# Kernel optimization log

Measured on AMD Instinct MI355X. Metric: run time of the kernel, lower is better.

Reference implementation:

```python
import jax, jax.numpy as jnp
import numpy as np

NEG_SLOPE = 0.01
H = 128  # hidden_conv_1 == hidden_conv_2


def leaky(x):
    return jnp.where(x >= 0, x, NEG_SLOPE * x)


def gru_cell(x, h, w_ih, w_hh, b_ih, b_hh):
    # PyTorch GRUCell: gates stacked [r, z, n] along dim 0 of w_ih/w_hh
    gi = x @ w_ih.T + b_ih  # [N, 3H]
    gh = h @ w_hh.T + b_hh
    ir, iz, inn = jnp.split(gi, 3, axis=-1)
    hr, hz, hn = jnp.split(gh, 3, axis=-1)
    r = jax.nn.sigmoid(ir + hr)
    z = jax.nn.sigmoid(iz + hz)
    n = jnp.tanh(inn + r * hn)
    return (1.0 - z) * n + z * h


def gcn_conv(x, w, b, src, dst, num_nodes):
    # PyG GCNConv: add self-loops, symmetric normalization, linear first
    xw = x @ w.T  # [N, H]
    loop = jnp.arange(num_nodes, dtype=src.dtype)
    s = jnp.concatenate([src, loop])
    d = jnp.concatenate([dst, loop])
    deg = jax.ops.segment_sum(jnp.ones_like(d, dtype=x.dtype), d, num_segments=num_nodes)
    dinv = jnp.where(deg > 0, jax.lax.rsqrt(deg), 0.0)
    norm = dinv[s] * dinv[d]  # [E+N]
    msg = xw[s] * norm[:, None]
    out = jax.ops.segment_sum(msg, d, num_segments=num_nodes)
    return out + b


def setup_inputs() -> dict:
    key = jax.random.key(0)
    ks = jax.random.split(key, 24)
    N, E, EL, IN_DIM, OUT_DIM = 100000, 600000, 200000, 128, 2

    def lin(k, fan_in, fan_out):
        k1, k2 = jax.random.split(k)
        bound = 1.0 / np.sqrt(fan_in)
        w = jax.random.uniform(k1, (fan_out, fan_in), minval=-bound, maxval=bound, dtype=jnp.float32)
        b = jax.random.uniform(k2, (fan_out,), minval=-bound, maxval=bound, dtype=jnp.float32)
        return w, b

    w_pre1, b_pre1 = lin(ks[0], IN_DIM, 256)
    w_pre2, b_pre2 = lin(ks[1], 256, H)
    w_c1, b_c1 = lin(ks[2], H, H)
    w_c2, b_c2 = lin(ks[3], H, H)
    w_post, b_post = lin(ks[4], H, OUT_DIM)

    def gru_params(k):
        k1, k2, k3, k4 = jax.random.split(k, 4)
        bound = 1.0 / np.sqrt(H)
        u = lambda kk, shape: jax.random.uniform(kk, shape, minval=-bound, maxval=bound, dtype=jnp.float32)
        return u(k1, (3 * H, H)), u(k2, (3 * H, H)), u(k3, (3 * H,)), u(k4, (3 * H,))

    g1_wih, g1_whh, g1_bih, g1_bhh = gru_params(ks[5])
    g2_wih, g2_whh, g2_bih, g2_bhh = gru_params(ks[6])

    x = jax.random.normal(ks[7], (N, IN_DIM), dtype=jnp.float32)
    edge_index = jax.random.randint(ks[8], (2, E), 0, N, dtype=jnp.int64 if jax.config.jax_enable_x64 else jnp.int32)
    edge_label_index = jax.random.randint(ks[9], (2, EL), 0, N, dtype=edge_index.dtype)
    prev_emb0 = jax.random.normal(ks[10], (N, H), dtype=jnp.float32)
    prev_emb1 = jax.random.normal(ks[11], (N, H), dtype=jnp.float32)

    return {
        'x': x, 'edge_index': edge_index, 'edge_label_index': edge_label_index,
        'prev_emb0': prev_emb0, 'prev_emb1': prev_emb1,
        'w_pre1': w_pre1, 'b_pre1': b_pre1, 'w_pre2': w_pre2, 'b_pre2': b_pre2,
        'w_c1': w_c1, 'b_c1': b_c1, 'w_c2': w_c2, 'b_c2': b_c2,
        'w_post': w_post, 'b_post': b_post,
        'g1_wih': g1_wih, 'g1_whh': g1_whh, 'g1_bih': g1_bih, 'g1_bhh': g1_bhh,
        'g2_wih': g2_wih, 'g2_whh': g2_whh, 'g2_bih': g2_bih, 'g2_bhh': g2_bhh,
    }


def reference(x, edge_index, edge_label_index, prev_emb0, prev_emb1,
              w_pre1, b_pre1, w_pre2, b_pre2, w_c1, b_c1, w_c2, b_c2,
              w_post, b_post, g1_wih, g1_whh, g1_bih, g1_bhh,
              g2_wih, g2_whh, g2_bih, g2_bhh):
    N = x.shape[0]
    src, dst = edge_index[0], edge_index[1]

    # preprocess (dropout p=0.0 -> identity)
    h = leaky(x @ w_pre1.T + b_pre1)
    h = leaky(h @ w_pre2.T + b_pre2)

    # unconditional GRU fuse with previous 0-hop embedding (detached in torch)
    h = jax.lax.stop_gradient(gru_cell(h, prev_emb0, g1_wih, g1_whh, g1_bih, g1_bhh))
    emb0 = h

    h = leaky(gcn_conv(h, w_c1, b_c1, src, dst, N))
    h = jax.lax.stop_gradient(gru_cell(h, prev_emb0, g1_wih, g1_whh, g1_bih, g1_bhh))
    emb1 = h

    h = leaky(gcn_conv(h, w_c2, b_c2, src, dst, N))
    h = jax.lax.stop_gradient(gru_cell(h, prev_emb1, g2_wih, g2_whh, g2_bih, g2_bhh))
    emb2 = h

    # LP head: gather + hadamard + linear + sum
    h_src = h[edge_label_index[0]]
    h_dst = h[edge_label_index[1]]
    logits = jnp.sum((h_src * h_dst) @ w_post.T + b_post, axis=-1)  # [EL]
    return logits, emb0, emb1, emb2
```

## Files before the change

### kernel.cpp

```cpp
#include <hip/hip_runtime.h>
#include <hip/hip_bf16.h>
#include <type_traits>


typedef __bf16 bf16;
typedef __bf16 bf16x8 __attribute__((ext_vector_type(8)));
typedef float  f32x4  __attribute__((ext_vector_type(4)));

#define DEV __device__ __forceinline__

DEV f32x4 mfma16(bf16x8 a, bf16x8 b, f32x4 c) {
    return __builtin_amdgcn_mfma_f32_16x16x32_bf16(a, b, c, 0, 0, 0);
}

DEV bf16x8 load_a8(const float* p) {
    f32x4 lo = *(const f32x4*)p;
    f32x4 hi = *(const f32x4*)(p + 4);
    bf16x8 v;
    v[0] = (bf16)lo[0]; v[1] = (bf16)lo[1]; v[2] = (bf16)lo[2]; v[3] = (bf16)lo[3];
    v[4] = (bf16)hi[0]; v[5] = (bf16)hi[1]; v[6] = (bf16)hi[2]; v[7] = (bf16)hi[3];
    return v;
}
DEV bf16x8 load_a8(const bf16* p) { return *(const bf16x8*)p; }

__global__ void cvt_kernel(const float* __restrict__ in, bf16* __restrict__ ob, int n) {
    const int i = blockIdx.x * 256 + threadIdx.x;
    if (i < n) ob[i] = (bf16)in[i];
}

template<int Ci, int Co, bool ACT, bool BIAS, typename AT, typename OT>
__global__ __launch_bounds__(256) void gemm_kernel(
    const AT* __restrict__ A, const bf16* __restrict__ W,
    const float* __restrict__ bias, OT* __restrict__ C, int M)
{
    const int tid  = threadIdx.x;
    const int lane = tid & 63, w = tid >> 6;
    const int lr   = lane & 15, ko = lane >> 4;
    const int rbase = blockIdx.x * 64 + w * 16;

    long arow = rbase + lr; if (arow > M - 1) arow = M - 1;
    constexpr int KC = Ci / 32;
    constexpr int NT = Co / 16;

    bf16x8 a[KC];
#pragma unroll
    for (int kc = 0; kc < KC; ++kc)
        a[kc] = load_a8(A + arow * Ci + kc * 32 + ko * 8);

#pragma unroll
    for (int t = 0; t < NT; ++t) {
        f32x4 acc = {0.f, 0.f, 0.f, 0.f};
        const bf16* wp = W + (long)(t * 16 + lr) * Ci + ko * 8;
#pragma unroll
        for (int kc = 0; kc < KC; ++kc)
            acc = mfma16(a[kc], *(const bf16x8*)(wp + kc * 32), acc);

        const int col = t * 16 + lr;
        float bv = 0.f;
        if (BIAS) bv = bias[col];
#pragma unroll
        for (int j = 0; j < 4; ++j) {
            const int orow = rbase + ko * 4 + j;
            if (orow < M) {
                float v = acc[j] + bv;
                if (ACT) v = (v >= 0.f) ? v : 0.01f * v;
                C[(long)orow * Co + col] = (OT)v;
            }
        }
    }
}

template<typename XT>
__global__ __launch_bounds__(256) void gru_kernel(
    const XT* x, const float* __restrict__ hp,
    const bf16* __restrict__ wih, const bf16* __restrict__ whh,
    const float* __restrict__ bih, const float* __restrict__ bhh,
    float* out, int N)
{
    __shared__ bf16 Lw[6][16][128];

    const int tid  = threadIdx.x;
    const int lane = tid & 63, w = tid >> 6;
    const int lr   = lane & 15, ko = lane >> 4;
    const long rbase = (long)blockIdx.x * 64 + w * 16;

    long arow = rbase + lr; if (arow > N - 1) arow = N - 1;
    bf16x8 ax[4], ah[4];
#pragma unroll
    for (int kc = 0; kc < 4; ++kc) {
        ax[kc] = load_a8(x  + arow * 128 + kc * 32 + ko * 8);
        ah[kc] = load_a8(hp + arow * 128 + kc * 32 + ko * 8);
    }

    for (int tc = 0; tc < 8; ++tc) {
        __syncthreads();
#pragma unroll
        for (int i = 0; i < 6; ++i) {
            const int ch  = tid + 256 * i;
            const int g   = ch >> 8, rem = ch & 255;
            const int row = rem >> 4, cc = rem & 15;
            const int scc = cc ^ (row & 7);
            const bf16* wsrc = (g < 3 ? wih : whh)
                + (long)(((g % 3) * 128 + tc * 16 + row) * 128 + scc * 8);
            *(bf16x8*)(&Lw[g][row][cc * 8]) = *(const bf16x8*)wsrc;
        }
        __syncthreads();

        const int col = tc * 16 + lr;
        const float br = bih[col]       + bhh[col];
        const float bz = bih[128 + col] + bhh[128 + col];
        const float bi = bih[256 + col];
        const float bh = bhh[256 + col];

        f32x4 ar = {0.f, 0.f, 0.f, 0.f};
        f32x4 az = {0.f, 0.f, 0.f, 0.f};
        f32x4 ai = {0.f, 0.f, 0.f, 0.f};
        f32x4 ag = {0.f, 0.f, 0.f, 0.f};
#pragma unroll
        for (int kc = 0; kc < 4; ++kc) {
            const int cc = (kc * 4 + ko) ^ (lr & 7);
            bf16x8 wr_i = *(const bf16x8*)(&Lw[0][lr][cc * 8]);
            bf16x8 wz_i = *(const bf16x8*)(&Lw[1][lr][cc * 8]);
            bf16x8 wn_i = *(const bf16x8*)(&Lw[2][lr][cc * 8]);
            bf16x8 wr_h = *(const bf16x8*)(&Lw[3][lr][cc * 8]);
            bf16x8 wz_h = *(const bf16x8*)(&Lw[4][lr][cc * 8]);
            bf16x8 wn_h = *(const bf16x8*)(&Lw[5][lr][cc * 8]);
            ar = mfma16(ax[kc], wr_i, ar);
            ar = mfma16(ah[kc], wr_h, ar);
            az = mfma16(ax[kc], wz_i, az);
            az = mfma16(ah[kc], wz_h, az);
            ai = mfma16(ax[kc], wn_i, ai);
            ag = mfma16(ah[kc], wn_h, ag);
        }
#pragma unroll
        for (int j = 0; j < 4; ++j) {
            const long row = rbase + ko * 4 + j;
            if (row < N) {
                const float r = 1.f / (1.f + __expf(-(ar[j] + br)));
                const float z = 1.f / (1.f + __expf(-(az[j] + bz)));
                const float pre = (ai[j] + bi) + r * (ag[j] + bh);
                const float n = 1.f - 2.f / (1.f + __expf(2.f * pre));
                out[row * 128 + col] = (1.f - z) * n + z * hp[row * 128 + col];
            }
        }
    }
}

__global__ void deg_kernel(const int* __restrict__ dst, int* degi, int E) {
    const int e = blockIdx.x * 256 + threadIdx.x;
    if (e < E) atomicAdd(&degi[dst[e]], 1);
}

__global__ void dinv_kernel(const int* __restrict__ degi, float* __restrict__ dinv, int N) {
    const int i = blockIdx.x * 256 + threadIdx.x;
    if (i < N) dinv[i] = rsqrtf((float)degi[i] + 1.0f);
}

__global__ void scan1_kernel(const int* __restrict__ degi, int* __restrict__ inc,
                             int* __restrict__ bsum, int N) {
    __shared__ int s[256];
    const int i = blockIdx.x * 256 + threadIdx.x;
    s[threadIdx.x] = (i < N) ? degi[i] : 0;
    __syncthreads();
#pragma unroll
    for (int off = 1; off < 256; off <<= 1) {
        int t = (threadIdx.x >= off) ? s[threadIdx.x - off] : 0;
        __syncthreads();
        s[threadIdx.x] += t;
        __syncthreads();
    }
    if (i < N) inc[i] = s[threadIdx.x];
    if (threadIdx.x == 255) bsum[blockIdx.x] = s[255];
}

__global__ void scan2_kernel(int* bsum, int nb) {
    __shared__ int s[512];
    __shared__ int carry;
    if (threadIdx.x == 0) carry = 0;
    __syncthreads();
    for (int base = 0; base < nb; base += 512) {
        const int i = base + threadIdx.x;
        s[threadIdx.x] = (i < nb) ? bsum[i] : 0;
        __syncthreads();
#pragma unroll
        for (int off = 1; off < 512; off <<= 1) {
            int t = (threadIdx.x >= off) ? s[threadIdx.x - off] : 0;
            __syncthreads();
            s[threadIdx.x] += t;
            __syncthreads();
        }
        const int c = carry;
        if (i < nb) bsum[i] = s[threadIdx.x] + c;
        __syncthreads();
        if (threadIdx.x == 511) carry = c + s[511];
        __syncthreads();
    }
}

__global__ void scan3_kernel(const int* __restrict__ inc, const int* __restrict__ degi,
                             const int* __restrict__ bsum, int* __restrict__ rowptr, int N) {
    const int i = blockIdx.x * 256 + threadIdx.x;
    if (i >= N) return;
    const int prev = (blockIdx.x > 0) ? bsum[blockIdx.x - 1] : 0;
    rowptr[i] = prev + inc[i] - degi[i];
}

__global__ void fill_kernel(const int* __restrict__ src, const int* __restrict__ dst,
                            const int* __restrict__ rowptr, int* cursor,
                            const float* __restrict__ dinv,
                            int* __restrict__ csr_src, float* __restrict__ csr_norm, int E) {
    const int e = blockIdx.x * 256 + threadIdx.x;
    if (e >= E) return;
    const int s = src[e], d = dst[e];
    const int pos = rowptr[d] + atomicAdd(&cursor[d], 1);
    csr_src[pos]  = s;
    csr_norm[pos] = dinv[s] * dinv[d];
}

template<typename OT>
__global__ __launch_bounds__(256) void gather_kernel(
    const bf16* __restrict__ xwb,
    const int* __restrict__ rowptr, const int* __restrict__ degi,
    const int* __restrict__ csr_src, const float* __restrict__ csr_norm,
    const float* __restrict__ dinv, const float* __restrict__ bias,
    OT* __restrict__ out, int N, int colbase, int cw, int lg)
{
    const long tid = (long)blockIdx.x * 256 + threadIdx.x;
    const long d = tid >> lg;
    const int  c = (int)(tid & ((1 << lg) - 1));
    if (d >= N) return;

    const int start = rowptr[d];
    const int deg   = degi[d];
    const int h     = deg >> 1;
    const bf16* xb  = xwb + c * 8;

    float acca[8] = {0.f, 0.f, 0.f, 0.f, 0.f, 0.f, 0.f, 0.f};
    float accb[8] = {0.f, 0.f, 0.f, 0.f, 0.f, 0.f, 0.f, 0.f};
    for (int k = 0; k < h; ++k) {
        const int   sa = csr_src[start + k];
        const int   sb = csr_src[start + h + k];
        const float na = csr_norm[start + k];
        const float nb_ = csr_norm[start + h + k];
        bf16x8 va = *(const bf16x8*)(xb + (long)sa * cw);
        bf16x8 vb = *(const bf16x8*)(xb + (long)sb * cw);
#pragma unroll
        for (int j = 0; j < 8; ++j) {
            acca[j] += (float)va[j] * na;
            accb[j] += (float)vb[j] * nb_;
        }
    }
    if (deg & 1) {
        const int   s  = csr_src[start + deg - 1];
        const float nm = csr_norm[start + deg - 1];
        bf16x8 v = *(const bf16x8*)(xb + (long)s * cw);
#pragma unroll
        for (int j = 0; j < 8; ++j) acca[j] += (float)v[j] * nm;
    }

    const float di = dinv[d], sl = di * di;
    bf16x8 vd = *(const bf16x8*)(xb + d * cw);
    const int col = colbase + c * 8;
    float v[8];
#pragma unroll
    for (int j = 0; j < 8; ++j) {
        float t = acca[j] + accb[j] + (float)vd[j] * sl + bias[col + j];
        v[j] = (t >= 0.f) ? t : 0.01f * t;
    }
    if constexpr (std::is_same<OT, bf16>::value) {
        bf16x8 o;
#pragma unroll
        for (int j = 0; j < 8; ++j) o[j] = (bf16)v[j];
        *(bf16x8*)(out + d * 128 + col) = o;
    } else {
        f32x4 o0, o1;
#pragma unroll
        for (int j = 0; j < 4; ++j) { o0[j] = v[j]; o1[j] = v[4 + j]; }
        *(f32x4*)(out + d * 128 + col)     = o0;
        *(f32x4*)(out + d * 128 + col + 4) = o1;
    }
}

__global__ __launch_bounds__(256) void lp_kernel(
    const float* __restrict__ emb, const int* __restrict__ eli,
    const float* __restrict__ wpost, const float* __restrict__ bpost,
    float* __restrict__ logits, int EL)
{
    const int e = blockIdx.x * 256 + threadIdx.x;
    if (e >= EL) return;
    const long s = eli[e], d = eli[EL + e];
    float acc = 0.f;
#pragma unroll
    for (int c = 0; c < 32; ++c) {
        f32x4 vs = *(const f32x4*)(emb + s * 128 + c * 4);
        f32x4 vd = *(const f32x4*)(emb + d * 128 + c * 4);
        f32x4 w0 = *(const f32x4*)(wpost + c * 4);
        f32x4 w1 = *(const f32x4*)(wpost + 128 + c * 4);
#pragma unroll
        for (int i = 0; i < 4; ++i)
            acc += vs[i] * vd[i] * (w0[i] + w1[i]);
    }
    logits[e] = acc + bpost[0] + bpost[1];
}

extern "C" void kernel_launch(void* const* d_in, const int* in_sizes, int n_in,
                              void* d_out, int out_size, void* d_ws, size_t ws_size,
                              hipStream_t stream) {
    const float* x      = (const float*)d_in[0];
    const int*   ei     = (const int*)d_in[1];
    const int*   eli    = (const int*)d_in[2];
    const float* prev0  = (const float*)d_in[3];
    const float* prev1  = (const float*)d_in[4];
    const float* w_pre1 = (const float*)d_in[5];
    const float* b_pre1 = (const float*)d_in[6];
    const float* w_pre2 = (const float*)d_in[7];
    const float* b_pre2 = (const float*)d_in[8];
    const float* w_c1   = (const float*)d_in[9];
    const float* b_c1   = (const float*)d_in[10];
    const float* w_c2   = (const float*)d_in[11];
    const float* b_c2   = (const float*)d_in[12];
    const float* w_post = (const float*)d_in[13];
    const float* b_post = (const float*)d_in[14];
    const float* g1_wih = (const float*)d_in[15];
    const float* g1_whh = (const float*)d_in[16];
    const float* g1_bih = (const float*)d_in[17];
    const float* g1_bhh = (const float*)d_in[18];
    const float* g2_wih = (const float*)d_in[19];
    const float* g2_whh = (const float*)d_in[20];
    const float* g2_bih = (const float*)d_in[21];
    const float* g2_bhh = (const float*)d_in[22];

    const int N  = in_sizes[0] / 128;
    const int E  = in_sizes[1] / 2;
    const int EL = in_sizes[2] / 2;
    const long NH = (long)N * 128;

    float* out    = (float*)d_out;
    float* logits = out;
    float* emb0   = out + EL;
    float* emb1   = emb0 + NH;
    float* emb2   = emb1 + NH;

    bf16* H1b = (bf16*)emb1;
    bf16* H2b = (bf16*)emb2;
    bf16* h1b = (bf16*)emb2;

    char* ws = (char*)d_ws;
    size_t p = 0;
    auto alloc = [&](size_t bytes) { size_t o = p; p = (p + bytes + 255) & ~(size_t)255; return o; };
    float* dinv    = (float*)(ws + alloc((size_t)N * 4));
    int*   degi    = (int*)  (ws + alloc((size_t)N * 4));
    int*   inc     = (int*)  (ws + alloc((size_t)N * 4));
    int*   rowptr  = (int*)  (ws + alloc((size_t)N * 4));
    int*   cursor  = (int*)  (ws + alloc((size_t)N * 4));
    int*   bsum    = (int*)  (ws + alloc(4096));
    bf16*  wb      = (bf16*) (ws + alloc((size_t)294912 * 2));
    int*   csr_src = (int*)  (ws + alloc((size_t)E * 4));
    float* csr_nrm = (float*)(ws + alloc((size_t)E * 4));
    const size_t fixed = p;
    bf16*  xwb     = (bf16*)(ws + fixed);

    int cw = 128;
    while (cw > 16 && fixed + (size_t)N * cw * 2 > ws_size) cw >>= 1;
    const int lg = __builtin_ctz(cw >> 3);
    const int passes = 128 / cw;

    const bool big_ws = (cw == 128) &&
        (ws_size >= fixed + (size_t)N * 128 * 2 + (size_t)N * 128 * 2);
    bf16* h2b = big_ws ? (bf16*)(ws + fixed + (size_t)N * 128 * 2) : nullptr;

    bf16* wb_pre1 = wb;
    bf16* wb_pre2 = wb_pre1 + 32768;
    bf16* wb_c1   = wb_pre2 + 32768;
    bf16* wb_c2   = wb_c1 + 16384;
    bf16* wb_g1i  = wb_c2 + 16384;
    bf16* wb_g1h  = wb_g1i + 49152;
    bf16* wb_g2i  = wb_g1h + 49152;
    bf16* wb_g2h  = wb_g2i + 49152;

    const int gB = 256;
    const dim3 blk(gB);
    const int grid_rows64 = (N + 63) / 64;
    const int grid_gru    = (N + 63) / 64;
    const int grid_E      = (E + gB - 1) / gB;
    const int grid_N      = (N + gB - 1) / gB;
    const int nb          = (N + 255) / 256;

    cvt_kernel<<<(32768 + 255) / 256, blk, 0, stream>>>(w_pre1, wb_pre1, 32768);
    cvt_kernel<<<(32768 + 255) / 256, blk, 0, stream>>>(w_pre2, wb_pre2, 32768);
    cvt_kernel<<<(16384 + 255) / 256, blk, 0, stream>>>(w_c1, wb_c1, 16384);
    cvt_kernel<<<(16384 + 255) / 256, blk, 0, stream>>>(w_c2, wb_c2, 16384);
    cvt_kernel<<<(49152 + 255) / 256, blk, 0, stream>>>(g1_wih, wb_g1i, 49152);
    cvt_kernel<<<(49152 + 255) / 256, blk, 0, stream>>>(g1_whh, wb_g1h, 49152);
    cvt_kernel<<<(49152 + 255) / 256, blk, 0, stream>>>(g2_wih, wb_g2i, 49152);
    cvt_kernel<<<(49152 + 255) / 256, blk, 0, stream>>>(g2_whh, wb_g2h, 49152);

    hipMemsetAsync(degi, 0, (size_t)N * 4, stream);
    deg_kernel<<<grid_E, blk, 0, stream>>>(ei + E, degi, E);
    dinv_kernel<<<grid_N, blk, 0, stream>>>(degi, dinv, N);
    scan1_kernel<<<nb, blk, 0, stream>>>(degi, inc, bsum, N);
    scan2_kernel<<<1, 512, 0, stream>>>(bsum, nb);
    scan3_kernel<<<nb, blk, 0, stream>>>(inc, degi, bsum, rowptr, N);
    hipMemsetAsync(cursor, 0, (size_t)N * 4, stream);
    fill_kernel<<<grid_E, blk, 0, stream>>>(ei, ei + E, rowptr, cursor, dinv, csr_src, csr_nrm, E);

    gemm_kernel<128, 256, true, true, float, bf16><<<grid_rows64, blk, 0, stream>>>(x, wb_pre1, b_pre1, H1b, N);
    gemm_kernel<256, 128, true, true, bf16,  bf16><<<grid_rows64, blk, 0, stream>>>(H1b, wb_pre2, b_pre2, H2b, N);

    gru_kernel<bf16><<<grid_gru, blk, 0, stream>>>(H2b, prev0, wb_g1i, wb_g1h, g1_bih, g1_bhh, emb0, N);

    const int grid_ga = (int)((((long)N << lg) + gB - 1) / gB);
    auto run_gemm = [&](const float* hin, const bf16* wp) {
        switch (cw) {
        case 128: gemm_kernel<128, 128, false, false, float, bf16><<<grid_rows64, blk, 0, stream>>>(hin, wp, nullptr, xwb, N); break;
        case 64:  gemm_kernel<128, 64,  false, false, float, bf16><<<grid_rows64, blk, 0, stream>>>(hin, wp, nullptr, xwb, N); break;
        case 32:  gemm_kernel<128, 32,  false, false, float, bf16><<<grid_rows64, blk, 0, stream>>>(hin, wp, nullptr, xwb, N); break;
        default:  gemm_kernel<128, 16,  false, false, float, bf16><<<grid_rows64, blk, 0, stream>>>(hin, wp, nullptr, xwb, N); break;
        }
    };

    for (int ps = 0; ps < passes; ++ps) {
        run_gemm(emb0, wb_c1 + (size_t)(ps * cw) * 128);
        gather_kernel<bf16><<<grid_ga, blk, 0, stream>>>(xwb, rowptr, degi, csr_src, csr_nrm,
                                                         dinv, b_c1, h1b, N, ps * cw, cw, lg);
    }
    gru_kernel<bf16><<<grid_gru, blk, 0, stream>>>(h1b, prev0, wb_g1i, wb_g1h, g1_bih, g1_bhh, emb1, N);

    for (int ps = 0; ps < passes; ++ps) {
        run_gemm(emb1, wb_c2 + (size_t)(ps * cw) * 128);
        if (big_ws)
            gather_kernel<bf16><<<grid_ga, blk, 0, stream>>>(xwb, rowptr, degi, csr_src, csr_nrm,
                                                             dinv, b_c2, h2b, N, ps * cw, cw, lg);
        else
            gather_kernel<float><<<grid_ga, blk, 0, stream>>>(xwb, rowptr, degi, csr_src, csr_nrm,
                                                              dinv, b_c2, emb2, N, ps * cw, cw, lg);
    }
    if (big_ws)
        gru_kernel<bf16><<<grid_gru, blk, 0, stream>>>(h2b, prev1, wb_g2i, wb_g2h, g2_bih, g2_bhh, emb2, N);
    else
        gru_kernel<float><<<grid_gru, blk, 0, stream>>>(emb2, prev1, wb_g2i, wb_g2h, g2_bih, g2_bhh, emb2, N);

    lp_kernel<<<(EL + gB - 1) / gB, blk, 0, stream>>>(emb2, eli, w_post, b_post, logits, EL);
}
```

Before: 588.3 us.

## Merge conversion and setup kernels, double-row GEMM tiles, prefetch GRU weights

Replaces the eight weight-conversion launches with one kernel and folds the dinv computation into the first scan kernel. The CSR fill now uses a copy of rowptr as its atomic cursor, which removes a memset and a load. The GEMM processes two 16-row tiles per wave so each weight fragment is reused twice, with half as many blocks. The GRU kernel prefetches the next weight tile into registers before computing on the current one. Together these aim to cut launch overhead and weight-load latency, at the cost of more register pressure and fewer blocks.

```diff
diff --git a/kernel.cpp b/kernel.cpp
--- a/kernel.cpp
+++ b/kernel.cpp
@@ -23,9 +23,21 @@
 }
 DEV bf16x8 load_a8(const bf16* p) { return *(const bf16x8*)p; }
 
-__global__ void cvt_kernel(const float* __restrict__ in, bf16* __restrict__ ob, int n) {
+__global__ void cvt8_kernel(const float* s0, const float* s1, const float* s2, const float* s3,
+                            const float* s4, const float* s5, const float* s6, const float* s7,
+                            bf16* __restrict__ wb) {
     const int i = blockIdx.x * 256 + threadIdx.x;
-    if (i < n) ob[i] = (bf16)in[i];
+    if (i >= 294912) return;
+    float v;
+    if      (i < 32768)  v = s0[i];
+    else if (i < 65536)  v = s1[i - 32768];
+    else if (i < 81920)  v = s2[i - 65536];
+    else if (i < 98304)  v = s3[i - 81920];
+    else if (i < 147456) v = s4[i - 98304];
+    else if (i < 196608) v = s5[i - 147456];
+    else if (i < 245760) v = s6[i - 196608];
+    else                 v = s7[i - 245760];
+    wb[i] = (bf16)v;
 }
 
 template<int Ci, int Co, bool ACT, bool BIAS, typename AT, typename OT>
@@ -36,35 +48,48 @@
     const int tid  = threadIdx.x;
     const int lane = tid & 63, w = tid >> 6;
     const int lr   = lane & 15, ko = lane >> 4;
-    const int rbase = blockIdx.x * 64 + w * 16;
-
-    long arow = rbase + lr; if (arow > M - 1) arow = M - 1;
+    const int rbase = blockIdx.x * 128 + w * 32;
+
     constexpr int KC = Ci / 32;
     constexpr int NT = Co / 16;
 
-    bf16x8 a[KC];
-#pragma unroll
-    for (int kc = 0; kc < KC; ++kc)
-        a[kc] = load_a8(A + arow * Ci + kc * 32 + ko * 8);
+    bf16x8 a[2][KC];
+#pragma unroll
+    for (int m = 0; m < 2; ++m) {
+        long arow = rbase + m * 16 + lr; if (arow > M - 1) arow = M - 1;
+#pragma unroll
+        for (int kc = 0; kc < KC; ++kc)
+            a[m][kc] = load_a8(A + arow * Ci + kc * 32 + ko * 8);
+    }
 
 #pragma unroll
     for (int t = 0; t < NT; ++t) {
-        f32x4 acc = {0.f, 0.f, 0.f, 0.f};
+        f32x4 acc0 = {0.f, 0.f, 0.f, 0.f};
+        f32x4 acc1 = {0.f, 0.f, 0.f, 0.f};
         const bf16* wp = W + (long)(t * 16 + lr) * Ci + ko * 8;
 #pragma unroll
-        for (int kc = 0; kc < KC; ++kc)
-            acc = mfma16(a[kc], *(const bf16x8*)(wp + kc * 32), acc);
+        for (int kc = 0; kc < KC; ++kc) {
+            bf16x8 wf = *(const bf16x8*)(wp + kc * 32);
+            acc0 = mfma16(a[0][kc], wf, acc0);
+            acc1 = mfma16(a[1][kc], wf, acc1);
+        }
 
         const int col = t * 16 + lr;
         float bv = 0.f;
         if (BIAS) bv = bias[col];
 #pragma unroll
         for (int j = 0; j < 4; ++j) {
-            const int orow = rbase + ko * 4 + j;
-            if (orow < M) {
-                float v = acc[j] + bv;
+            const int r0 = rbase + ko * 4 + j;
+            if (r0 < M) {
+                float v = acc0[j] + bv;
                 if (ACT) v = (v >= 0.f) ? v : 0.01f * v;
-                C[(long)orow * Co + col] = (OT)v;
+                C[(long)r0 * Co + col] = (OT)v;
+            }
+            const int r1 = rbase + 16 + ko * 4 + j;
+            if (r1 < M) {
+                float v = acc1[j] + bv;
+                if (ACT) v = (v >= 0.f) ? v : 0.01f * v;
+                C[(long)r1 * Co + col] = (OT)v;
             }
         }
     }
@@ -92,19 +117,31 @@
         ah[kc] = load_a8(hp + arow * 128 + kc * 32 + ko * 8);
     }
 
-    for (int tc = 0; tc < 8; ++tc) {
-        __syncthreads();
+    bf16x8 pre[6];
+    auto LDW = [&](int tc) {
 #pragma unroll
         for (int i = 0; i < 6; ++i) {
             const int ch  = tid + 256 * i;
             const int g   = ch >> 8, rem = ch & 255;
             const int row = rem >> 4, cc = rem & 15;
             const int scc = cc ^ (row & 7);
-            const bf16* wsrc = (g < 3 ? wih : whh)
-                + (long)(((g % 3) * 128 + tc * 16 + row) * 128 + scc * 8);
-            *(bf16x8*)(&Lw[g][row][cc * 8]) = *(const bf16x8*)wsrc;
-        }
-        __syncthreads();
+            pre[i] = *(const bf16x8*)((g < 3 ? wih : whh)
+                + (long)(((g % 3) * 128 + tc * 16 + row) * 128 + scc * 8));
+        }
+    };
+    LDW(0);
+
+    for (int tc = 0; tc < 8; ++tc) {
+        __syncthreads();
+#pragma unroll
+        for (int i = 0; i < 6; ++i) {
+            const int ch  = tid + 256 * i;
+            const int g   = ch >> 8, rem = ch & 255;
+            const int row = rem >> 4, cc = rem & 15;
+            *(bf16x8*)(&Lw[g][row][cc * 8]) = pre[i];
+        }
+        __syncthreads();
+        if (tc < 7) LDW(tc + 1);
 
         const int col = tc * 16 + lr;
         const float br = bih[col]       + bhh[col];
@@ -138,8 +175,8 @@
             if (row < N) {
                 const float r = 1.f / (1.f + __expf(-(ar[j] + br)));
                 const float z = 1.f / (1.f + __expf(-(az[j] + bz)));
-                const float pre = (ai[j] + bi) + r * (ag[j] + bh);
-                const float n = 1.f - 2.f / (1.f + __expf(2.f * pre));
+                const float pre_ = (ai[j] + bi) + r * (ag[j] + bh);
+                const float n = 1.f - 2.f / (1.f + __expf(2.f * pre_));
                 out[row * 128 + col] = (1.f - z) * n + z * hp[row * 128 + col];
             }
         }
@@ -151,16 +188,13 @@
     if (e < E) atomicAdd(&degi[dst[e]], 1);
 }
 
-__global__ void dinv_kernel(const int* __restrict__ degi, float* __restrict__ dinv, int N) {
-    const int i = blockIdx.x * 256 + threadIdx.x;
-    if (i < N) dinv[i] = rsqrtf((float)degi[i] + 1.0f);
-}
-
 __global__ void scan1_kernel(const int* __restrict__ degi, int* __restrict__ inc,
-                             int* __restrict__ bsum, int N) {
+                             int* __restrict__ bsum, float* __restrict__ dinv, int N) {
     __shared__ int s[256];
     const int i = blockIdx.x * 256 + threadIdx.x;
-    s[threadIdx.x] = (i < N) ? degi[i] : 0;
+    const int d = (i < N) ? degi[i] : 0;
+    if (i < N) dinv[i] = rsqrtf((float)d + 1.0f);
+    s[threadIdx.x] = d;
     __syncthreads();
 #pragma unroll
     for (int off = 1; off < 256; off <<= 1) {
@@ -198,21 +232,23 @@
 }
 
 __global__ void scan3_kernel(const int* __restrict__ inc, const int* __restrict__ degi,
-                             const int* __restrict__ bsum, int* __restrict__ rowptr, int N) {
+                             const int* __restrict__ bsum, int* __restrict__ rowptr,
+                             int* __restrict__ rp2, int N) {
     const int i = blockIdx.x * 256 + threadIdx.x;
     if (i >= N) return;
     const int prev = (blockIdx.x > 0) ? bsum[blockIdx.x - 1] : 0;
-    rowptr[i] = prev + inc[i] - degi[i];
+    const int rp = prev + inc[i] - degi[i];
+    rowptr[i] = rp;
+    rp2[i]    = rp;
 }
 
 __global__ void fill_kernel(const int* __restrict__ src, const int* __restrict__ dst,
-                            const int* __restrict__ rowptr, int* cursor,
-                            const float* __restrict__ dinv,
+                            int* rp2, const float* __restrict__ dinv,
                             int* __restrict__ csr_src, float* __restrict__ csr_norm, int E) {
     const int e = blockIdx.x * 256 + threadIdx.x;
     if (e >= E) return;
     const int s = src[e], d = dst[e];
-    const int pos = rowptr[d] + atomicAdd(&cursor[d], 1);
+    const int pos = atomicAdd(&rp2[d], 1);
     csr_src[pos]  = s;
     csr_norm[pos] = dinv[s] * dinv[d];
 }
@@ -352,7 +388,7 @@
     int*   degi    = (int*)  (ws + alloc((size_t)N * 4));
     int*   inc     = (int*)  (ws + alloc((size_t)N * 4));
     int*   rowptr  = (int*)  (ws + alloc((size_t)N * 4));
-    int*   cursor  = (int*)  (ws + alloc((size_t)N * 4));
+    int*   rp2     = (int*)  (ws + alloc((size_t)N * 4));
     int*   bsum    = (int*)  (ws + alloc(4096));
     bf16*  wb      = (bf16*) (ws + alloc((size_t)294912 * 2));
     int*   csr_src = (int*)  (ws + alloc((size_t)E * 4));
@@ -380,42 +416,33 @@
 
     const int gB = 256;
     const dim3 blk(gB);
-    const int grid_rows64 = (N + 63) / 64;
-    const int grid_gru    = (N + 63) / 64;
-    const int grid_E      = (E + gB - 1) / gB;
-    const int grid_N      = (N + gB - 1) / gB;
-    const int nb          = (N + 255) / 256;
-
-    cvt_kernel<<<(32768 + 255) / 256, blk, 0, stream>>>(w_pre1, wb_pre1, 32768);
-    cvt_kernel<<<(32768 + 255) / 256, blk, 0, stream>>>(w_pre2, wb_pre2, 32768);
-    cvt_kernel<<<(16384 + 255) / 256, blk, 0, stream>>>(w_c1, wb_c1, 16384);
-    cvt_kernel<<<(16384 + 255) / 256, blk, 0, stream>>>(w_c2, wb_c2, 16384);
-    cvt_kernel<<<(49152 + 255) / 256, blk, 0, stream>>>(g1_wih, wb_g1i, 49152);
-    cvt_kernel<<<(49152 + 255) / 256, blk, 0, stream>>>(g1_whh, wb_g1h, 49152);
-    cvt_kernel<<<(49152 + 255) / 256, blk, 0, stream>>>(g2_wih, wb_g2i, 49152);
-    cvt_kernel<<<(49152 + 255) / 256, blk, 0, stream>>>(g2_whh, wb_g2h, 49152);
+    const int grid_rows128 = (N + 127) / 128;
+    const int grid_gru     = (N + 63) / 64;
+    const int grid_E       = (E + gB - 1) / gB;
+    const int nb           = (N + 255) / 256;
+
+    cvt8_kernel<<<(294912 + 255) / 256, blk, 0, stream>>>(
+        w_pre1, w_pre2, w_c1, w_c2, g1_wih, g1_whh, g2_wih, g2_whh, wb);
 
     hipMemsetAsync(degi, 0, (size_t)N * 4, stream);
     deg_kernel<<<grid_E, blk, 0, stream>>>(ei + E, degi, E);
-    dinv_kernel<<<grid_N, blk, 0, stream>>>(degi, dinv, N);
-    scan1_kernel<<<nb, blk, 0, stream>>>(degi, inc, bsum, N);
+    scan1_kernel<<<nb, blk, 0, stream>>>(degi, inc, bsum, dinv, N);
     scan2_kernel<<<1, 512, 0, stream>>>(bsum, nb);
-    scan3_kernel<<<nb, blk, 0, stream>>>(inc, degi, bsum, rowptr, N);
-    hipMemsetAsync(cursor, 0, (size_t)N * 4, stream);
-    fill_kernel<<<grid_E, blk, 0, stream>>>(ei, ei + E, rowptr, cursor, dinv, csr_src, csr_nrm, E);
-
-    gemm_kernel<128, 256, true, true, float, bf16><<<grid_rows64, blk, 0, stream>>>(x, wb_pre1, b_pre1, H1b, N);
-    gemm_kernel<256, 128, true, true, bf16,  bf16><<<grid_rows64, blk, 0, stream>>>(H1b, wb_pre2, b_pre2, H2b, N);
+    scan3_kernel<<<nb, blk, 0, stream>>>(inc, degi, bsum, rowptr, rp2, N);
+    fill_kernel<<<grid_E, blk, 0, stream>>>(ei, ei + E, rp2, dinv, csr_src, csr_nrm, E);
+
+    gemm_kernel<128, 256, true, true, float, bf16><<<grid_rows128, blk, 0, stream>>>(x, wb_pre1, b_pre1, H1b, N);
+    gemm_kernel<256, 128, true, true, bf16,  bf16><<<grid_rows128, blk, 0, stream>>>(H1b, wb_pre2, b_pre2, H2b, N);
 
     gru_kernel<bf16><<<grid_gru, blk, 0, stream>>>(H2b, prev0, wb_g1i, wb_g1h, g1_bih, g1_bhh, emb0, N);
 
     const int grid_ga = (int)((((long)N << lg) + gB - 1) / gB);
     auto run_gemm = [&](const float* hin, const bf16* wp) {
         switch (cw) {
-        case 128: gemm_kernel<128, 128, false, false, float, bf16><<<grid_rows64, blk, 0, stream>>>(hin, wp, nullptr, xwb, N); break;
-        case 64:  gemm_kernel<128, 64,  false, false, float, bf16><<<grid_rows64, blk, 0, stream>>>(hin, wp, nullptr, xwb, N); break;
-        case 32:  gemm_kernel<128, 32,  false, false, float, bf16><<<grid_rows64, blk, 0, stream>>>(hin, wp, nullptr, xwb, N); break;
-        default:  gemm_kernel<128, 16,  false, false, float, bf16><<<grid_rows64, blk, 0, stream>>>(hin, wp, nullptr, xwb, N); break;
+        case 128: gemm_kernel<128, 128, false, false, float, bf16><<<grid_rows128, blk, 0, stream>>>(hin, wp, nullptr, xwb, N); break;
+        case 64:  gemm_kernel<128, 64,  false, false, float, bf16><<<grid_rows128, blk, 0, stream>>>(hin, wp, nullptr, xwb, N); break;
+        case 32:  gemm_kernel<128, 32,  false, false, float, bf16><<<grid_rows128, blk, 0, stream>>>(hin, wp, nullptr, xwb, N); break;
+        default:  gemm_kernel<128, 16,  false, false, float, bf16><<<grid_rows128, blk, 0, stream>>>(hin, wp, nullptr, xwb, N); break;
         }
     };
 
```

Result: faster. 545.4 us (-7.3%).
